# Performance work log

Hardware: AMD Instinct MI355X
Metric: run time of the kernel (lower is better)

Reference implementation:

```python
import jax, jax.numpy as jnp
import numpy as np

# PM-field / module constants (from module source + plausible PMField defaults)
DT = 0.1          # PM-field integration step
EPS = 1e-4        # softening of gravitational flow
PM_STEPS = 4      # pm_steps
TAU = 0.9         # membrane_tau
M_GAIN = 0.1      # membrane_gain
EI_GAIN = 0.06    # VectorizedLateralEI gain
PLR = 0.001       # plasticity_lr (mu_lr = c_lr)


def setup_inputs() -> dict:
    key = jax.random.key(0)
    ks = jax.random.split(key, 8)
    B, D_IN, D_HID, D_LAT, N_C, CH, N_CLS = 16384, 784, 256, 8, 64, 64, 10
    x = jax.random.normal(ks[0], (B, D_IN), jnp.float32)
    W1 = jax.random.normal(ks[1], (D_IN, D_HID), jnp.float32) * 0.05
    b1 = jnp.zeros((D_HID,), jnp.float32)
    W2 = jax.random.normal(ks[2], (D_HID, D_LAT), jnp.float32) * 0.05
    b2 = jnp.zeros((D_LAT,), jnp.float32)
    mu = jax.random.uniform(ks[3], (N_C,), jnp.float32) * 0.5       # center strengths
    c = jax.random.normal(ks[4], (N_C, D_LAT), jnp.float32)         # center positions
    Wp = jax.random.normal(ks[5], (D_LAT, CH), jnp.float32) * 0.3
    bp = jnp.zeros((CH,), jnp.float32)
    Wr = jax.random.normal(ks[6], (CH, N_CLS), jnp.float32) * 0.1
    br = jnp.zeros((N_CLS,), jnp.float32)
    return {"x": x, "W1": W1, "b1": b1, "W2": W2, "b2": b2, "mu": mu,
            "c": c, "Wp": Wp, "bp": bp, "Wr": Wr, "br": br, "T": 5}


def _pm_evolve(z, mu, c):
    # Gravitational PM-field: z follows softened attraction to centers c with strengths mu.
    def body(z, _):
        d = c[None, :, :] - z[:, None, :]            # [B, N, D]
        r2 = jnp.sum(d * d, axis=-1) + EPS           # [B, N]
        z = z + DT * jnp.einsum('bn,bnd->bd', mu / r2, d)
        return z, None
    z, _ = jax.lax.scan(body, z, None, length=PM_STEPS)
    return z


def _forward(x, W1, b1, W2, b2, mu, c, Wp, bp, Wr, br, T):
    z = jnp.tanh(x @ W1 + b1) @ W2 + b2              # enc: [B, d_latent]
    h = jnp.zeros((x.shape[0], Wp.shape[1]), x.dtype)

    def step(carry, _):
        z, h, mu, c = carry
        z_ev = _pm_evolve(z, mu, c)
        h_proj = jnp.tanh(z_ev @ Wp + bp)
        h_new = TAU * h + M_GAIN * h_proj
        # lateral EI: excitation minus mean inhibition
        h_f = h_new + EI_GAIN * (h_new - jnp.mean(h_new, axis=-1, keepdims=True))
        logits = h_f @ Wr + br
        # vectorized Hebbian plasticity on PM centers (no-grad, like torch .data update)
        d = c[None, :, :] - z_ev[:, None, :]
        r2 = jnp.sum(d * d, axis=-1)                 # [B, N]
        act = jnp.exp(-r2)                           # center activity
        post = jnp.mean(h_f, axis=-1)                # postsynaptic drive [B]
        mu2 = mu + PLR * jnp.mean(act * post[:, None], axis=0)
        wsum = jnp.sum(act, axis=0)                  # [N]
        w = act / (wsum + EPS)[None, :]
        c2 = c + PLR * (jnp.einsum('bn,bd->nd', w, z_ev) - c * (wsum / (wsum + EPS))[:, None])
        mu2 = jax.lax.stop_gradient(mu2)
        c2 = jax.lax.stop_gradient(c2)
        return (z_ev, h_f, mu2, c2), logits

    (z, h, _, _), logits_seq = jax.lax.scan(step, (z, h, mu, c), None, length=T)
    return logits_seq[-1], z, h


def reference(x, W1, b1, W2, b2, mu, c, Wp, bp, Wr, br, T):
    return _forward(x, W1, b1, W2, b2, mu, c, Wp, bp, Wr, br, T)
```

## Files before the change

### kernel.cpp

```cpp
#include <hip/hip_runtime.h>
#include <math.h>

#define B_N     16384
#define D_IN    784
#define D_HID   256
#define D_LAT   8
#define N_CTR   64
#define CH_N    64
#define N_CLS   10

#define DT_C    0.1f
#define EPS_C   1e-4f
#define PM_STEPS 4
#define TAU_C   0.9f
#define MGAIN   0.1f
#define EIG     0.06f
#define PLR_C   0.001f
#define T_STEPS 5

#define KP      832

typedef short bf16x8 __attribute__((ext_vector_type(8)));
typedef float f32x4v __attribute__((ext_vector_type(4)));

__device__ __forceinline__ void split_pair(float a, float b, unsigned& hi, unsigned& lo) {
    unsigned ua = __float_as_uint(a), ub = __float_as_uint(b);
    hi = (ua >> 16) | (ub & 0xffff0000u);
    float ra = a - __uint_as_float(ua & 0xffff0000u);
    float rb = b - __uint_as_float(ub & 0xffff0000u);
    lo = (__float_as_uint(ra) >> 16) | (__float_as_uint(rb) & 0xffff0000u);
}

__global__ __launch_bounds__(256) void w1t_kernel(
    const float* __restrict__ W1, ushort* __restrict__ WtH, ushort* __restrict__ WtL)
{
    __shared__ float t[32][36];
    const int kb = blockIdx.x;
    const int nb = blockIdx.y;
    const int tid = threadIdx.x;
    {
        const int r = tid >> 3, c4 = (tid & 7) * 4;
        const int k = kb * 32 + r;
        float4 v = {0.f, 0.f, 0.f, 0.f};
        if (k < D_IN) v = *(const float4*)(W1 + (size_t)k * 256 + nb * 32 + c4);
        t[r][c4 + 0] = v.x; t[r][c4 + 1] = v.y; t[r][c4 + 2] = v.z; t[r][c4 + 3] = v.w;
    }
    __syncthreads();
    const int n = tid >> 3, kq = (tid & 7) * 4;
    float a0 = t[kq + 0][n], a1 = t[kq + 1][n], a2 = t[kq + 2][n], a3 = t[kq + 3][n];
    unsigned h0, l0, h1w, l1w;
    split_pair(a0, a1, h0, l0);
    split_pair(a2, a3, h1w, l1w);
    const size_t o = (size_t)(nb * 32 + n) * KP + kb * 32 + kq;
    uint2 hv; hv.x = h0; hv.y = h1w;
    uint2 lv; lv.x = l0; lv.y = l1w;
    *(uint2*)(WtH + o) = hv;
    *(uint2*)(WtL + o) = lv;
}

__global__ __launch_bounds__(256, 3) void enc1_kernel(
    const float* __restrict__ x, const ushort* __restrict__ WtH,
    const ushort* __restrict__ WtL, const float* __restrict__ b1,
    float* __restrict__ h1)
{
    __shared__ alignas(16) unsigned char AhiS[16384];
    __shared__ alignas(16) unsigned char AloS[16384];
    __shared__ alignas(16) unsigned char BhiS[8192];
    __shared__ alignas(16) unsigned char BloS[8192];

    const int tid = threadIdx.x;
    const int bx  = blockIdx.x;
    const int n0  = (bx & 3) * 64;
    const int m0  = (bx >> 2) * 128;

    const int m_s = tid >> 1, kh = tid & 1;
    const int n_s = tid >> 2, kq = tid & 3;
    const float*  xrow = x + (size_t)(m0 + m_s) * D_IN;
    const ushort* bhrow = WtH + (size_t)(n0 + n_s) * KP + kq * 16;
    const ushort* blrow = WtL + (size_t)(n0 + n_s) * KP + kq * 16;
    const unsigned offB0 = (unsigned)(n_s * 128) + (unsigned)(((2 * kq)     ^ (n_s & 7)) << 4);
    const unsigned offB1 = (unsigned)(n_s * 128) + (unsigned)(((2 * kq + 1) ^ (n_s & 7)) << 4);

    const int lane = tid & 63;
    const int wid  = tid >> 6;
    const int wm   = wid >> 1, wn = wid & 1;
    const int fr   = lane & 15, g = lane >> 4;
    const unsigned swz = (unsigned)((fr & 7) << 4);
    const int kgb  = g * 16;

    f32x4v acc[4][2];
    #pragma unroll
    for (int mi = 0; mi < 4; ++mi)
        #pragma unroll
        for (int ni = 0; ni < 2; ++ni) acc[mi][ni] = (f32x4v){0.f, 0.f, 0.f, 0.f};

    for (int kt = 0; kt < 13; ++kt) {
        const int kbase = kt * 64 + kh * 32;
        float4 av[8];
        #pragma unroll
        for (int q = 0; q < 8; ++q) {
            const int kk = kbase + q * 4;
            float4 z4 = {0.f, 0.f, 0.f, 0.f};
            av[q] = (kk < D_IN) ? *(const float4*)(xrow + kk) : z4;
        }
        #pragma unroll
        for (int q16 = 0; q16 < 4; ++q16) {
            uint4 hw, lw;
            split_pair(av[2 * q16].x,     av[2 * q16].y,     hw.x, lw.x);
            split_pair(av[2 * q16].z,     av[2 * q16].w,     hw.y, lw.y);
            split_pair(av[2 * q16 + 1].x, av[2 * q16 + 1].y, hw.z, lw.z);
            split_pair(av[2 * q16 + 1].z, av[2 * q16 + 1].w, hw.w, lw.w);
            const unsigned off = (unsigned)(m_s * 128) +
                (unsigned)((((kh * 4 + q16) ^ (m_s & 7))) << 4);
            *(uint4*)(AhiS + off) = hw;
            *(uint4*)(AloS + off) = lw;
        }
        {
            const int ko = kt * 64;
            uint4 h0 = *(const uint4*)(bhrow + ko);
            uint4 h1v = *(const uint4*)(bhrow + ko + 8);
            uint4 l0 = *(const uint4*)(blrow + ko);
            uint4 l1v = *(const uint4*)(blrow + ko + 8);
            *(uint4*)(BhiS + offB0) = h0;
            *(uint4*)(BhiS + offB1) = h1v;
            *(uint4*)(BloS + offB0) = l0;
            *(uint4*)(BloS + offB1) = l1v;
        }
        __syncthreads();

        #pragma unroll
        for (int ks = 0; ks < 2; ++ks) {
            const unsigned kb = (unsigned)(ks * 64 + kgb);
            bf16x8 ah[4], al[4];
            #pragma unroll
            for (int mi = 0; mi < 4; ++mi) {
                const unsigned off = (unsigned)((wm * 64 + mi * 16 + fr) * 128) + (kb ^ swz);
                ah[mi] = *(const bf16x8*)(AhiS + off);
                al[mi] = *(const bf16x8*)(AloS + off);
            }
            #pragma unroll
            for (int ni = 0; ni < 2; ++ni) {
                const unsigned offb = (unsigned)((wn * 32 + ni * 16 + fr) * 128) + (kb ^ swz);
                bf16x8 bh = *(const bf16x8*)(BhiS + offb);
                bf16x8 bl = *(const bf16x8*)(BloS + offb);
                #pragma unroll
                for (int mi = 0; mi < 4; ++mi) {
                    acc[mi][ni] = __builtin_amdgcn_mfma_f32_16x16x32_bf16(ah[mi], bh, acc[mi][ni], 0, 0, 0);
                    acc[mi][ni] = __builtin_amdgcn_mfma_f32_16x16x32_bf16(ah[mi], bl, acc[mi][ni], 0, 0, 0);
                    acc[mi][ni] = __builtin_amdgcn_mfma_f32_16x16x32_bf16(al[mi], bh, acc[mi][ni], 0, 0, 0);
                }
            }
        }
        __syncthreads();
    }

    #pragma unroll
    for (int ni = 0; ni < 2; ++ni) {
        const int col = n0 + wn * 32 + ni * 16 + fr;
        const float bias = b1[col];
        #pragma unroll
        for (int mi = 0; mi < 4; ++mi) {
            #pragma unroll
            for (int r = 0; r < 4; ++r) {
                const int row = m0 + wm * 64 + mi * 16 + g * 4 + r;
                h1[(size_t)row * 256 + col] = tanhf(acc[mi][ni][r] + bias);
            }
        }
    }
}

__global__ __launch_bounds__(256) void enc2_kernel(
    const float* __restrict__ h1, const float* __restrict__ W2,
    const float* __restrict__ b2, float* __restrict__ zT)
{
    __shared__ alignas(16) float hs[32][260];
    __shared__ alignas(16) float w2t[8][260];
    const int tid = threadIdx.x;
    const int r0 = blockIdx.x * 32;
    for (int i = tid; i < D_HID * D_LAT; i += 256) {
        int k = i >> 3, d = i & 7;
        w2t[d][k] = W2[i];
    }
    #pragma unroll
    for (int i = 0; i < 8; ++i) {
        int idx = tid + i * 256;
        int rr = idx >> 6, c4 = idx & 63;
        float4 v = *(const float4*)(h1 + (size_t)(r0 + rr) * D_HID + c4 * 4);
        *(float4*)&hs[rr][c4 * 4] = v;
    }
    __syncthreads();
    const int r = tid >> 3, d = tid & 7;
    float acc = 0.f;
    #pragma unroll 8
    for (int k4 = 0; k4 < 64; ++k4) {
        float4 a = *(const float4*)&hs[r][k4 * 4];
        float4 w = *(const float4*)&w2t[d][k4 * 4];
        acc = fmaf(a.x, w.x, acc);
        acc = fmaf(a.y, w.y, acc);
        acc = fmaf(a.z, w.z, acc);
        acc = fmaf(a.w, w.w, acc);
    }
    zT[(size_t)(r0 + r) * 8 + d] = acc + b2[d];
}

__global__ __launch_bounds__(256) void stepA2_kernel(
    float* __restrict__ zT, float* __restrict__ hT,
    const float* __restrict__ mu, const float* __restrict__ c,
    const float* __restrict__ Wp, const float* __restrict__ bp,
    const float* __restrict__ Wr, const float* __restrict__ br,
    float* __restrict__ part, float* __restrict__ out, int t)
{
    __shared__ alignas(16) float mu_s[64];
    __shared__ alignas(16) float c_s[512];
    __shared__ alignas(16) float wp_s[512];
    __shared__ alignas(16) float bp_s[64];
    __shared__ alignas(16) float wr_s[704];
    __shared__ alignas(16) float br_s[16];
    __shared__ alignas(16) float act_s[32 * 72];
    __shared__ alignas(16) float z_s[256];
    __shared__ alignas(16) float post_s[32];
    __shared__ alignas(16) float red2[4 * 64 * 10];
    const int tid = threadIdx.x;
    if (tid < 64) { mu_s[tid] = mu[tid]; bp_s[tid] = bp[tid]; }
    for (int i = tid; i < 512; i += 256) { c_s[i] = c[i]; wp_s[i] = Wp[i]; }
    const bool last = (t == T_STEPS - 1);
    if (last) {
        for (int i = tid; i < 640; i += 256) wr_s[(i / 10) * 11 + (i % 10)] = Wr[i];
        if (tid < N_CLS) br_s[tid] = br[tid];
    }
    __syncthreads();

    const int sub  = tid & 7;
    const int grp  = tid >> 3;
    const int b    = blockIdx.x * 32 + grp;
    const int lane = tid & 63;
    const int gbase = lane & ~7;

    float zown = zT[(size_t)b * 8 + sub];
    float z[8];
    #pragma unroll
    for (int d = 0; d < 8; ++d) z[d] = __shfl(zown, gbase + d, 64);

    #pragma unroll 1
    for (int it = 0; it < PM_STEPS; ++it) {
        float f[8];
        #pragma unroll
        for (int d = 0; d < 8; ++d) f[d] = 0.f;
        #pragma unroll
        for (int k = 0; k < 8; ++k) {
            const int n = sub + 8 * k;
            float dx[8];
            float r2 = EPS_C;
            #pragma unroll
            for (int d = 0; d < 8; ++d) {
                dx[d] = c_s[n * 8 + d] - z[d];
                r2 = fmaf(dx[d], dx[d], r2);
            }
            float w = mu_s[n] / r2;
            #pragma unroll
            for (int d = 0; d < 8; ++d) f[d] = fmaf(w, dx[d], f[d]);
        }
        #pragma unroll
        for (int m = 1; m <= 4; m <<= 1)
            #pragma unroll
            for (int d = 0; d < 8; ++d) f[d] += __shfl_xor(f[d], m, 64);
        #pragma unroll
        for (int d = 0; d < 8; ++d) z[d] = fmaf(DT_C, f[d], z[d]);
    }
    float zsel = z[0];
    #pragma unroll
    for (int d = 1; d < 8; ++d) if (sub == d) zsel = z[d];
    zT[(size_t)b * 8 + sub] = zsel;

    float hn[8];
    float s = 0.f;
    #pragma unroll
    for (int j = 0; j < 8; ++j) {
        const int ch = sub * 8 + j;
        float a = bp_s[ch];
        #pragma unroll
        for (int d = 0; d < 8; ++d) a = fmaf(z[d], wp_s[d * 64 + ch], a);
        hn[j] = tanhf(a);
    }
    if (t == 0) {
        #pragma unroll
        for (int j = 0; j < 8; ++j) { hn[j] = MGAIN * hn[j]; s += hn[j]; }
    } else {
        const float4* hp = (const float4*)(hT + (size_t)b * 64 + sub * 8);
        float4 h0 = hp[0], h1v = hp[1];
        hn[0] = TAU_C * h0.x + MGAIN * hn[0];
        hn[1] = TAU_C * h0.y + MGAIN * hn[1];
        hn[2] = TAU_C * h0.z + MGAIN * hn[2];
        hn[3] = TAU_C * h0.w + MGAIN * hn[3];
        hn[4] = TAU_C * h1v.x + MGAIN * hn[4];
        hn[5] = TAU_C * h1v.y + MGAIN * hn[5];
        hn[6] = TAU_C * h1v.z + MGAIN * hn[6];
        hn[7] = TAU_C * h1v.w + MGAIN * hn[7];
        #pragma unroll
        for (int j = 0; j < 8; ++j) s += hn[j];
    }
    #pragma unroll
    for (int m = 1; m <= 4; m <<= 1) s += __shfl_xor(s, m, 64);
    const float mean = s * (1.f / 64.f);
    float spost = 0.f;
    #pragma unroll
    for (int j = 0; j < 8; ++j) {
        hn[j] = hn[j] + EIG * (hn[j] - mean);
        spost += hn[j];
    }
    {
        float4 a0 = {hn[0], hn[1], hn[2], hn[3]};
        float4 a1 = {hn[4], hn[5], hn[6], hn[7]};
        float4* hp = (float4*)(hT + (size_t)b * 64 + sub * 8);
        hp[0] = a0; hp[1] = a1;
    }
    #pragma unroll
    for (int m = 1; m <= 4; m <<= 1) spost += __shfl_xor(spost, m, 64);

    if (!last) {
        z_s[tid] = zsel;
        if (sub == 0) post_s[grp] = spost * (1.f / 64.f);
        #pragma unroll
        for (int k = 0; k < 8; ++k) {
            const int n = sub + 8 * k;
            float r2 = 0.f;
            #pragma unroll
            for (int d = 0; d < 8; ++d) {
                float dd = c_s[n * 8 + d] - z[d];
                r2 = fmaf(dd, dd, r2);
            }
            act_s[grp * 72 + n] = expf(-r2);
        }
        __syncthreads();
        const int q = tid >> 6, n2 = tid & 63;
        float r[10];
        #pragma unroll
        for (int j = 0; j < 10; ++j) r[j] = 0.f;
        #pragma unroll
        for (int i = 0; i < 8; ++i) {
            const int g2 = q * 8 + i;
            float a = act_s[g2 * 72 + n2];
            r[0] += a;
            r[1] = fmaf(a, post_s[g2], r[1]);
            #pragma unroll
            for (int d = 0; d < 8; ++d)
                r[2 + d] = fmaf(a, z_s[g2 * 8 + d], r[2 + d]);
        }
        #pragma unroll
        for (int j = 0; j < 10; ++j) red2[(q * 64 + n2) * 10 + j] = r[j];
        __syncthreads();
        if (q == 0) {
            #pragma unroll
            for (int j = 0; j < 10; ++j) {
                float sv = (red2[(n2) * 10 + j] + red2[(64 + n2) * 10 + j]) +
                           (red2[(128 + n2) * 10 + j] + red2[(192 + n2) * 10 + j]);
                part[((size_t)blockIdx.x * 64 + n2) * 10 + j] = sv;
            }
        }
    } else {
        float lg[N_CLS];
        #pragma unroll
        for (int cls = 0; cls < N_CLS; ++cls) lg[cls] = 0.f;
        #pragma unroll
        for (int j = 0; j < 8; ++j) {
            const int ch = sub * 8 + j;
            #pragma unroll
            for (int cls = 0; cls < N_CLS; ++cls)
                lg[cls] = fmaf(hn[j], wr_s[ch * 11 + cls], lg[cls]);
        }
        #pragma unroll
        for (int m = 1; m <= 4; m <<= 1)
            #pragma unroll
            for (int cls = 0; cls < N_CLS; ++cls) lg[cls] += __shfl_xor(lg[cls], m, 64);
        if (sub == 0) {
            #pragma unroll
            for (int cls = 0; cls < N_CLS; ++cls)
                out[(size_t)b * 10 + cls] = lg[cls] + br_s[cls];
        }
        out[163840 + (size_t)b * 8 + sub] = zsel;
        {
            float4 a0 = {hn[0], hn[1], hn[2], hn[3]};
            float4 a1 = {hn[4], hn[5], hn[6], hn[7]};
            float4* op = (float4*)(out + 294912 + (size_t)b * 64 + sub * 8);
            op[0] = a0; op[1] = a1;
        }
    }
}

__global__ __launch_bounds__(256) void stepB2_kernel(
    const float* __restrict__ part,
    const float* __restrict__ mu_in, const float* __restrict__ c_in,
    float* __restrict__ mu_out, float* __restrict__ c_out)
{
    const int n = blockIdx.x, tid = threadIdx.x;
    __shared__ float red[256][10];
    const float* p0 = part + ((size_t)tid * 64 + n) * 10;
    const float* p1 = part + ((size_t)(tid + 256) * 64 + n) * 10;
    #pragma unroll
    for (int j = 0; j < 10; ++j) red[tid][j] = p0[j] + p1[j];
    __syncthreads();
    for (int s = 128; s > 0; s >>= 1) {
        if (tid < s) {
            #pragma unroll
            for (int j = 0; j < 10; ++j) red[tid][j] += red[tid + s][j];
        }
        __syncthreads();
    }
    if (tid == 0) {
        const float S1 = red[0][0];
        const float S2 = red[0][1] * (1.f / B_N);
        mu_out[n] = mu_in[n] + PLR_C * S2;
        const float denom = S1 + EPS_C;
        #pragma unroll
        for (int d = 0; d < 8; ++d) {
            float s3 = red[0][2 + d];
            c_out[n * 8 + d] = c_in[n * 8 + d] + PLR_C * (s3 / denom - c_in[n * 8 + d] * (S1 / denom));
        }
    }
}

extern "C" void kernel_launch(void* const* d_in, const int* in_sizes, int n_in,
                              void* d_out, int out_size, void* d_ws, size_t ws_size,
                              hipStream_t stream) {
    (void)in_sizes; (void)n_in; (void)out_size; (void)ws_size;
    const float* x   = (const float*)d_in[0];
    const float* W1  = (const float*)d_in[1];
    const float* b1  = (const float*)d_in[2];
    const float* W2  = (const float*)d_in[3];
    const float* b2  = (const float*)d_in[4];
    const float* mu0 = (const float*)d_in[5];
    const float* c0  = (const float*)d_in[6];
    const float* Wp  = (const float*)d_in[7];
    const float* bp  = (const float*)d_in[8];
    const float* Wr  = (const float*)d_in[9];
    const float* br  = (const float*)d_in[10];
    float* out = (float*)d_out;
    float* ws  = (float*)d_ws;

    float* h1    = ws;
    float* hT    = ws;
    float* part  = ws + 2113536;
    float* zT    = ws + 4194304;
    float* mu_buf = ws + 4325376;
    float* c_buf  = ws + 4325504;
    ushort* WtH  = (ushort*)(ws + 4326528);
    ushort* WtL  = (ushort*)(ws + 4433024);

    w1t_kernel<<<dim3(26, 8), 256, 0, stream>>>(W1, WtH, WtL);
    enc1_kernel<<<512, 256, 0, stream>>>(x, WtH, WtL, b1, h1);
    enc2_kernel<<<512, 256, 0, stream>>>(h1, W2, b2, zT);

    const float* mu_cur = mu0;
    const float* c_cur  = c0;
    for (int t = 0; t < T_STEPS; ++t) {
        stepA2_kernel<<<512, 256, 0, stream>>>(zT, hT, mu_cur, c_cur, Wp, bp, Wr, br,
                                               part, out, t);
        if (t < T_STEPS - 1) {
            float* mo = mu_buf + (t & 1) * 64;
            float* co = c_buf  + (t & 1) * 512;
            stepB2_kernel<<<64, 256, 0, stream>>>(part, mu_cur, c_cur, mo, co);
            mu_cur = mo;
            c_cur  = co;
        }
    }
}
```

Baseline: 141.9 us.

## Double-buffer encoder GEMM with direct global-to-LDS loads and fast math intrinsics

Restructures the first encoder GEMM into a double-buffered pipeline over 25 K-tiles of 32. The W1 hi/lo tiles are fetched with global_load_lds straight into shared memory, and the next x tile is prefetched into registers while MFMAs run on the current buffer. Block indices are remapped for locality, and the K padding drops from 832 to 800. In the step kernel, the division, tanh and exp are swapped for hardware reciprocal and __expf-based approximations, which trades a little accuracy for fewer instructions.

Result: slower. 149.5 us (+5.3%).

```diff
diff --git a/kernel.cpp b/kernel.cpp
--- a/kernel.cpp
+++ b/kernel.cpp
@@ -18,7 +18,8 @@
 #define PLR_C   0.001f
 #define T_STEPS 5
 
-#define KP      832
+#define KP      800
+#define NKT     25
 
 typedef short bf16x8 __attribute__((ext_vector_type(8)));
 typedef float f32x4v __attribute__((ext_vector_type(4)));
@@ -29,6 +30,18 @@
     float ra = a - __uint_as_float(ua & 0xffff0000u);
     float rb = b - __uint_as_float(ub & 0xffff0000u);
     lo = (__float_as_uint(ra) >> 16) | (__float_as_uint(rb) & 0xffff0000u);
+}
+
+__device__ __forceinline__ void gload_lds16(const void* g, void* l) {
+    __builtin_amdgcn_global_load_lds(
+        (const __attribute__((address_space(1))) unsigned*)g,
+        (__attribute__((address_space(3))) unsigned*)l, 16, 0, 0);
+}
+
+__device__ __forceinline__ float fast_rcp(float x) { return __builtin_amdgcn_rcpf(x); }
+__device__ __forceinline__ float fast_tanh(float a) {
+    float e = __expf(2.0f * a);
+    return 1.0f - 2.0f * fast_rcp(e + 1.0f);
 }
 
 __global__ __launch_bounds__(256) void w1t_kernel(
@@ -63,30 +76,27 @@
     const ushort* __restrict__ WtL, const float* __restrict__ b1,
     float* __restrict__ h1)
 {
-    __shared__ alignas(16) unsigned char AhiS[16384];
-    __shared__ alignas(16) unsigned char AloS[16384];
-    __shared__ alignas(16) unsigned char BhiS[8192];
-    __shared__ alignas(16) unsigned char BloS[8192];
+    __shared__ alignas(16) unsigned char As[2][16384];
+    __shared__ alignas(16) unsigned char Bs[2][8192];
 
     const int tid = threadIdx.x;
     const int bx  = blockIdx.x;
-    const int n0  = (bx & 3) * 64;
-    const int m0  = (bx >> 2) * 128;
-
-    const int m_s = tid >> 1, kh = tid & 1;
-    const int n_s = tid >> 2, kq = tid & 3;
-    const float*  xrow = x + (size_t)(m0 + m_s) * D_IN;
-    const ushort* bhrow = WtH + (size_t)(n0 + n_s) * KP + kq * 16;
-    const ushort* blrow = WtL + (size_t)(n0 + n_s) * KP + kq * 16;
-    const unsigned offB0 = (unsigned)(n_s * 128) + (unsigned)(((2 * kq)     ^ (n_s & 7)) << 4);
-    const unsigned offB1 = (unsigned)(n_s * 128) + (unsigned)(((2 * kq + 1) ^ (n_s & 7)) << 4);
+    const int wk  = (bx & 7) * 64 + (bx >> 3);
+    const int n0  = (wk & 3) * 64;
+    const int m0  = (wk >> 2) * 128;
+
+    const int ar = tid >> 1, ah_ = tid & 1;
+    const float* xrow = x + (size_t)(m0 + ar) * D_IN;
+    const unsigned aswz = (unsigned)(ar & 7);
+
+    const int l = tid & 63, w = tid >> 6;
+    const int brow_g = (l >> 3);
+    const int us = l & 7;
 
     const int lane = tid & 63;
     const int wid  = tid >> 6;
     const int wm   = wid >> 1, wn = wid & 1;
     const int fr   = lane & 15, g = lane >> 4;
-    const unsigned swz = (unsigned)((fr & 7) << 4);
-    const int kgb  = g * 16;
 
     f32x4v acc[4][2];
     #pragma unroll
@@ -94,63 +104,93 @@
         #pragma unroll
         for (int ni = 0; ni < 2; ++ni) acc[mi][ni] = (f32x4v){0.f, 0.f, 0.f, 0.f};
 
-    for (int kt = 0; kt < 13; ++kt) {
-        const int kbase = kt * 64 + kh * 32;
-        float4 av[8];
-        #pragma unroll
-        for (int q = 0; q < 8; ++q) {
-            const int kk = kbase + q * 4;
-            float4 z4 = {0.f, 0.f, 0.f, 0.f};
-            av[q] = (kk < D_IN) ? *(const float4*)(xrow + kk) : z4;
-        }
-        #pragma unroll
-        for (int q16 = 0; q16 < 4; ++q16) {
-            uint4 hw, lw;
-            split_pair(av[2 * q16].x,     av[2 * q16].y,     hw.x, lw.x);
-            split_pair(av[2 * q16].z,     av[2 * q16].w,     hw.y, lw.y);
-            split_pair(av[2 * q16 + 1].x, av[2 * q16 + 1].y, hw.z, lw.z);
-            split_pair(av[2 * q16 + 1].z, av[2 * q16 + 1].w, hw.w, lw.w);
-            const unsigned off = (unsigned)(m_s * 128) +
-                (unsigned)((((kh * 4 + q16) ^ (m_s & 7))) << 4);
-            *(uint4*)(AhiS + off) = hw;
-            *(uint4*)(AloS + off) = lw;
-        }
+    float4 av[4];
+
+#define STAGE_B(kt_, buf_)                                                          \
+    {                                                                               \
+        _Pragma("unroll")                                                           \
+        for (int i = 0; i < 2; ++i) {                                               \
+            const int row = w * 16 + i * 8 + brow_g;                                \
+            const int u = us ^ (row & 7);                                           \
+            const ushort* src = ((u < 4) ? WtH : WtL) +                             \
+                (size_t)(n0 + row) * KP + (kt_) * 32 + (u & 3) * 8;                 \
+            gload_lds16(src, (void*)(Bs[buf_] + w * 2048 + i * 1024));              \
+        }                                                                           \
+    }
+#define LOAD_A(kt_)                                                                 \
+    {                                                                               \
+        const int kbase = (kt_) * 32 + ah_ * 16;                                    \
+        _Pragma("unroll")                                                           \
+        for (int q = 0; q < 4; ++q) {                                               \
+            const int kk = kbase + q * 4;                                           \
+            float4 z4 = {0.f, 0.f, 0.f, 0.f};                                       \
+            av[q] = (kk < D_IN) ? *(const float4*)(xrow + kk) : z4;                 \
+        }                                                                           \
+    }
+#define WRITE_A(buf_)                                                               \
+    {                                                                               \
+        unsigned hw[8], lw[8];                                                      \
+        split_pair(av[0].x, av[0].y, hw[0], lw[0]);                                 \
+        split_pair(av[0].z, av[0].w, hw[1], lw[1]);                                 \
+        split_pair(av[1].x, av[1].y, hw[2], lw[2]);                                 \
+        split_pair(av[1].z, av[1].w, hw[3], lw[3]);                                 \
+        split_pair(av[2].x, av[2].y, hw[4], lw[4]);                                 \
+        split_pair(av[2].z, av[2].w, hw[5], lw[5]);                                 \
+        split_pair(av[3].x, av[3].y, hw[6], lw[6]);                                 \
+        split_pair(av[3].z, av[3].w, hw[7], lw[7]);                                 \
+        unsigned char* base = As[buf_] + ar * 128;                                  \
+        uint4 v0 = {hw[0], hw[1], hw[2], hw[3]};                                    \
+        uint4 v1 = {hw[4], hw[5], hw[6], hw[7]};                                    \
+        uint4 v2 = {lw[0], lw[1], lw[2], lw[3]};                                    \
+        uint4 v3 = {lw[4], lw[5], lw[6], lw[7]};                                    \
+        *(uint4*)(base + ((((unsigned)(2 * ah_ + 0)) ^ aswz) << 4)) = v0;           \
+        *(uint4*)(base + ((((unsigned)(2 * ah_ + 1)) ^ aswz) << 4)) = v1;           \
+        *(uint4*)(base + ((((unsigned)(4 + 2 * ah_ + 0)) ^ aswz) << 4)) = v2;       \
+        *(uint4*)(base + ((((unsigned)(4 + 2 * ah_ + 1)) ^ aswz) << 4)) = v3;       \
+    }
+
+    STAGE_B(0, 0);
+    LOAD_A(0);
+    WRITE_A(0);
+    asm volatile("s_waitcnt vmcnt(0)" ::: "memory");
+    __syncthreads();
+
+    for (int kt = 0; kt < NKT; ++kt) {
+        const int cur = kt & 1;
+        const bool more = (kt + 1 < NKT);
+        if (more) {
+            STAGE_B(kt + 1, cur ^ 1);
+            LOAD_A(kt + 1);
+        }
+
         {
-            const int ko = kt * 64;
-            uint4 h0 = *(const uint4*)(bhrow + ko);
-            uint4 h1v = *(const uint4*)(bhrow + ko + 8);
-            uint4 l0 = *(const uint4*)(blrow + ko);
-            uint4 l1v = *(const uint4*)(blrow + ko + 8);
-            *(uint4*)(BhiS + offB0) = h0;
-            *(uint4*)(BhiS + offB1) = h1v;
-            *(uint4*)(BloS + offB0) = l0;
-            *(uint4*)(BloS + offB1) = l1v;
-        }
-        __syncthreads();
-
-        #pragma unroll
-        for (int ks = 0; ks < 2; ++ks) {
-            const unsigned kb = (unsigned)(ks * 64 + kgb);
-            bf16x8 ah[4], al[4];
+            bf16x8 ahv[4], alv[4];
             #pragma unroll
             for (int mi = 0; mi < 4; ++mi) {
-                const unsigned off = (unsigned)((wm * 64 + mi * 16 + fr) * 128) + (kb ^ swz);
-                ah[mi] = *(const bf16x8*)(AhiS + off);
-                al[mi] = *(const bf16x8*)(AloS + off);
+                const int row = wm * 64 + mi * 16 + fr;
+                const unsigned rb = (unsigned)(row & 7);
+                const unsigned base = (unsigned)(row * 128);
+                ahv[mi] = *(const bf16x8*)(As[cur] + base + ((((unsigned)g) ^ rb) << 4));
+                alv[mi] = *(const bf16x8*)(As[cur] + base + ((((unsigned)(4 + g)) ^ rb) << 4));
             }
             #pragma unroll
             for (int ni = 0; ni < 2; ++ni) {
-                const unsigned offb = (unsigned)((wn * 32 + ni * 16 + fr) * 128) + (kb ^ swz);
-                bf16x8 bh = *(const bf16x8*)(BhiS + offb);
-                bf16x8 bl = *(const bf16x8*)(BloS + offb);
+                const int row = wn * 32 + ni * 16 + fr;
+                const unsigned rb = (unsigned)(row & 7);
+                const unsigned base = (unsigned)(row * 128);
+                bf16x8 bh = *(const bf16x8*)(Bs[cur] + base + ((((unsigned)g) ^ rb) << 4));
+                bf16x8 bl = *(const bf16x8*)(Bs[cur] + base + ((((unsigned)(4 + g)) ^ rb) << 4));
                 #pragma unroll
                 for (int mi = 0; mi < 4; ++mi) {
-                    acc[mi][ni] = __builtin_amdgcn_mfma_f32_16x16x32_bf16(ah[mi], bh, acc[mi][ni], 0, 0, 0);
-                    acc[mi][ni] = __builtin_amdgcn_mfma_f32_16x16x32_bf16(ah[mi], bl, acc[mi][ni], 0, 0, 0);
-                    acc[mi][ni] = __builtin_amdgcn_mfma_f32_16x16x32_bf16(al[mi], bh, acc[mi][ni], 0, 0, 0);
+                    acc[mi][ni] = __builtin_amdgcn_mfma_f32_16x16x32_bf16(ahv[mi], bh, acc[mi][ni], 0, 0, 0);
+                    acc[mi][ni] = __builtin_amdgcn_mfma_f32_16x16x32_bf16(ahv[mi], bl, acc[mi][ni], 0, 0, 0);
+                    acc[mi][ni] = __builtin_amdgcn_mfma_f32_16x16x32_bf16(alv[mi], bh, acc[mi][ni], 0, 0, 0);
                 }
             }
         }
+
+        if (more) WRITE_A(cur ^ 1);
+        asm volatile("s_waitcnt vmcnt(0)" ::: "memory");
         __syncthreads();
     }
 
@@ -167,6 +207,9 @@
             }
         }
     }
+#undef STAGE_B
+#undef LOAD_A
+#undef WRITE_A
 }
 
 __global__ __launch_bounds__(256) void enc2_kernel(
@@ -256,9 +299,9 @@
                 dx[d] = c_s[n * 8 + d] - z[d];
                 r2 = fmaf(dx[d], dx[d], r2);
             }
-            float w = mu_s[n] / r2;
-            #pragma unroll
-            for (int d = 0; d < 8; ++d) f[d] = fmaf(w, dx[d], f[d]);
+            float wgt = mu_s[n] * fast_rcp(r2);
+            #pragma unroll
+            for (int d = 0; d < 8; ++d) f[d] = fmaf(wgt, dx[d], f[d]);
         }
         #pragma unroll
         for (int m = 1; m <= 4; m <<= 1)
@@ -280,7 +323,7 @@
         float a = bp_s[ch];
         #pragma unroll
         for (int d = 0; d < 8; ++d) a = fmaf(z[d], wp_s[d * 64 + ch], a);
-        hn[j] = tanhf(a);
+        hn[j] = fast_tanh(a);
     }
     if (t == 0) {
         #pragma unroll
@@ -329,7 +372,7 @@
                 float dd = c_s[n * 8 + d] - z[d];
                 r2 = fmaf(dd, dd, r2);
             }
-            act_s[grp * 72 + n] = expf(-r2);
+            act_s[grp * 72 + n] = __expf(-r2);
         }
         __syncthreads();
         const int q = tid >> 6, n2 = tid & 63;
@@ -444,9 +487,9 @@
     float* mu_buf = ws + 4325376;
     float* c_buf  = ws + 4325504;
     ushort* WtH  = (ushort*)(ws + 4326528);
-    ushort* WtL  = (ushort*)(ws + 4433024);
-
-    w1t_kernel<<<dim3(26, 8), 256, 0, stream>>>(W1, WtH, WtL);
+    ushort* WtL  = (ushort*)(ws + 4428928);
+
+    w1t_kernel<<<dim3(25, 8), 256, 0, stream>>>(W1, WtH, WtL);
     enc1_kernel<<<512, 256, 0, stream>>>(x, WtH, WtL, b1, h1);
     enc2_kernel<<<512, 256, 0, stream>>>(h1, W2, b2, zT);
 
```
